# Kernel optimization log

Hardware: AMD Instinct MI355X
Metric: run time of the kernel (lower is better)

The kernel has to match this reference:

```python
import jax, jax.numpy as jnp
import numpy as np

K, D_AMB, D_LAT = 16, 512, 10   # k clusters, ambient dim D, latent dim d
B = 16384                       # batch size
LAMB = 0.01                     # objective regularization weight (default)


def setup_inputs() -> dict:
    key = jax.random.key(0)
    k1, k2, k3 = jax.random.split(key, 3)
    std = 0.1 / np.sqrt(D_AMB)  # reset_parameters: normal(0, 0.1/sqrt(D))
    x = jax.random.normal(k1, (B, D_AMB), dtype=jnp.float32)
    Us = (jax.random.normal(k2, (K, D_AMB, D_LAT), dtype=jnp.float32) * std)
    Vs = (jax.random.normal(k3, (K, D_LAT, D_AMB), dtype=jnp.float32) * std)
    return {"x": x, "Us": Us, "Vs": Vs}


def reference(x, Us, Vs):
    # encode: z[k,b,:] = Vs[k] @ x[b]          (k, B, d)
    z = jnp.einsum('kdD,bD->kbd', Vs, x)
    # decode: x_[k,b,:] = Us[k] @ z[k,b]       (k, B, D)
    x_ = jnp.einsum('kDd,kbd->kbD', Us, z)
    # l2_sqr reconstruction loss, reduced over D, transposed to (B, k)
    diff = x[None, :, :] - x_
    loss = jnp.sum(diff * diff, axis=2).T                      # (B, K)
    # subspace regularization per cluster
    reg = 0.5 * (jnp.sum(Us ** 2, axis=(1, 2))
                 + jnp.sum(Vs ** 2, axis=(1, 2)))              # (K,)
    # hard assignment (soft_assign=0): one-hot argmin of detached assign_obj
    assign_obj = jax.lax.stop_gradient(loss + LAMB * reg[None, :])
    c = jax.nn.one_hot(jnp.argmin(assign_obj, axis=1), K, dtype=loss.dtype)
    # objective: mean over batch of c-weighted loss + lamb * c-weighted reg
    loss_term = jnp.mean(jnp.sum(c * loss, axis=1))
    reg_term = LAMB * jnp.mean(jnp.sum(c * reg[None, :], axis=1))
    return loss_term + reg_term
```

## Files before the change

### kernel.cpp

```cpp
#include <hip/hip_runtime.h>


#define KCLUST   16
#define DAMB     512
#define DLAT     10
#define BATCH    16384
#define LAMBDA   0.01f

#define BM       64
#define NTHREADS 512
#define NKS      16
#define NNT      20
#define NBLK     (BATCH / BM)
#define CHB      40960
#define SSTR     84

typedef __attribute__((ext_vector_type(8))) short short8;
typedef __attribute__((ext_vector_type(4))) float f32x4;

__device__ inline short f2bf(float f) {
    unsigned u = __builtin_bit_cast(unsigned, f);
    unsigned r = (u + 0x7FFFu + ((u >> 16) & 1u)) >> 16;
    return (short)r;
}

__global__ __launch_bounds__(256) void setup_k(const float* __restrict__ Us,
                                               const float* __restrict__ Vs,
                                               short* __restrict__ wpack,
                                               float* __restrict__ G,
                                               float* __restrict__ lreg,
                                               unsigned* __restrict__ cnt) {
    int b = blockIdx.x;
    int tid = threadIdx.x;
    if (b == 0 && tid == 0)
        __hip_atomic_store(cnt, 0u, __ATOMIC_RELEASE, __HIP_MEMORY_SCOPE_AGENT);
    if (b < 80) {
        int idx  = b * 256 + tid;
        int ks   = idx / (NNT * 64);
        int rem  = idx % (NNT * 64);
        int nt   = rem / 64;
        int lane = rem % 64;
        int col  = nt * 16 + (lane & 15);
        int cl   = col / 20;
        int c    = col % 20;
        short8 sv;
#pragma unroll
        for (int j = 0; j < 8; ++j) {
            int k = ks * 32 + (lane >> 4) * 8 + j;
            float v;
            if (c < DLAT) v = Vs[(size_t)cl * DLAT * DAMB + c * DAMB + k];
            else          v = Us[(size_t)cl * DAMB * DLAT + k * DLAT + (c - DLAT)];
            sv[j] = f2bf(v);
        }
        *(short8*)&wpack[(size_t)idx * 8] = sv;
    } else {
        __shared__ float red[256];
        int k = b - 80;
        const float* Uk = Us + (size_t)k * DAMB * DLAT;
        const float* Vk = Vs + (size_t)k * DLAT * DAMB;
        float s = 0.f;
        for (int i = tid; i < DAMB * DLAT; i += 256) {
            float a = Uk[i], bb = Vk[i];
            s += a * a + bb * bb;
        }
        red[tid] = s;
        __syncthreads();
        for (int st = 128; st > 0; st >>= 1) {
            if (tid < st) red[tid] += red[tid + st];
            __syncthreads();
        }
        if (tid == 0) lreg[k] = LAMBDA * 0.5f * red[0];
        if (tid < DLAT * DLAT) {
            int i = tid / DLAT, j = tid % DLAT;
            float g = 0.f;
            for (int Dv = 0; Dv < DAMB; ++Dv)
                g += Uk[Dv * DLAT + i] * Uk[Dv * DLAT + j];
            G[k * 100 + tid] = g;
        }
    }
}

__device__ __forceinline__ void gload_lds16(const void* g, void* l) {
    __builtin_amdgcn_global_load_lds(
        (const __attribute__((address_space(1))) unsigned int*)g,
        (__attribute__((address_space(3))) unsigned int*)l, 16, 0, 0);
}

template <int N> __device__ __forceinline__ void waitv() {
    if constexpr (N == 0)      asm volatile("s_waitcnt vmcnt(0)" ::: "memory");
    else if constexpr (N == 5) asm volatile("s_waitcnt vmcnt(5)" ::: "memory");
    __builtin_amdgcn_sched_barrier(0);
}

__global__ __launch_bounds__(NTHREADS) void main_k(const float* __restrict__ x,
                                                   const short* __restrict__ wpack,
                                                   const float* __restrict__ G,
                                                   const float* __restrict__ lreg,
                                                   float* __restrict__ parts,
                                                   unsigned* __restrict__ cnt,
                                                   float* __restrict__ out) {
    __shared__ __align__(16) char a_region[65536];
    __shared__ __align__(16) char b_region[2 * CHB];
    __shared__ float Gs[KCLUST * 100];
    __shared__ float lregs[KCLUST];
    __shared__ float rsqp[BM][8];
    __shared__ float rowsq_s[BM];
    __shared__ int   isLast;

    short* a_lds = (short*)a_region;
    float* sbuf  = (float*)a_region;
    float (*objl)[17] = (float(*)[17])b_region;

    const int tid  = threadIdx.x;
    const int lane = tid & 63;
    const int wv   = tid >> 6;
    const int mw   = wv >> 2;
    const int nw   = wv & 3;
    const int row0 = blockIdx.x * BM;

    {
        const int srow = tid >> 3;
        const int sc   = tid & 7;
        const int mt   = srow >> 4;
        const int rlo  = srow & 15;
        const float* xr = x + (size_t)(row0 + srow) * DAMB;
        float rs = 0.f;
#pragma unroll
        for (int i = 0; i < 8; ++i) {
            int k8 = sc + 8 * i;
            float4 v0 = *(const float4*)(xr + k8 * 8);
            float4 v1 = *(const float4*)(xr + k8 * 8 + 4);
            rs += v0.x * v0.x + v0.y * v0.y + v0.z * v0.z + v0.w * v0.w
                + v1.x * v1.x + v1.y * v1.y + v1.z * v1.z + v1.w * v1.w;
            short8 sv;
            sv[0] = f2bf(v0.x); sv[1] = f2bf(v0.y); sv[2] = f2bf(v0.z); sv[3] = f2bf(v0.w);
            sv[4] = f2bf(v1.x); sv[5] = f2bf(v1.y); sv[6] = f2bf(v1.z); sv[7] = f2bf(v1.w);
            int ks = k8 >> 2, lh = k8 & 3;
            int ln = (lh << 4) | rlo;
            *(short8*)&a_lds[((mt * NKS + ks) * 64 + ln) * 8] = sv;
        }
        rsqp[srow][sc] = rs;
    }
    for (int i = tid; i < KCLUST * 100; i += NTHREADS) Gs[i] = G[i];
    if (tid < KCLUST) lregs[tid] = lreg[tid];
    __syncthreads();
    if (tid < BM) {
        float s = 0.f;
#pragma unroll
        for (int j = 0; j < 8; ++j) s += rsqp[tid][j];
        rowsq_s[tid] = s;
    }

    f32x4 acc[2][5];
#pragma unroll
    for (int m = 0; m < 2; ++m)
#pragma unroll
        for (int j = 0; j < 5; ++j) acc[m][j] = (f32x4)0.f;

    const char* wsrc = (const char*)wpack;
    const int soff = (wv * 5) * 1024 + lane * 16;

#define ISSUE(c) do { \
        const char* s_ = wsrc + (size_t)(c) * CHB + soff; \
        char* d_ = b_region + ((c) & 1) * CHB + soff; \
        gload_lds16(s_ + 0,    d_ + 0); \
        gload_lds16(s_ + 1024, d_ + 1024); \
        gload_lds16(s_ + 2048, d_ + 2048); \
        gload_lds16(s_ + 3072, d_ + 3072); \
        gload_lds16(s_ + 4096, d_ + 4096); \
        __builtin_amdgcn_sched_barrier(0); \
    } while (0)

#define KSTEP(c, VM) do { \
        waitv<VM>(); \
        __builtin_amdgcn_s_barrier(); \
        __builtin_amdgcn_sched_barrier(0); \
        const short* B_ = (const short*)(b_region + ((c) & 1) * CHB); \
        _Pragma("unroll") \
        for (int ksl = 0; ksl < 2; ++ksl) { \
            short8 a0 = *(short8*)&a_lds[(((mw * 2 + 0) * NKS + (c) * 2 + ksl) * 64 + lane) * 8]; \
            short8 a1 = *(short8*)&a_lds[(((mw * 2 + 1) * NKS + (c) * 2 + ksl) * 64 + lane) * 8]; \
            _Pragma("unroll") \
            for (int j = 0; j < 5; ++j) { \
                short8 bf = *(short8*)&B_[((ksl * NNT + nw * 5 + j) * 64 + lane) * 8]; \
                acc[0][j] = __builtin_amdgcn_mfma_f32_16x16x32_bf16(a0, bf, acc[0][j], 0, 0, 0); \
                acc[1][j] = __builtin_amdgcn_mfma_f32_16x16x32_bf16(a1, bf, acc[1][j], 0, 0, 0); \
            } \
        } \
        __builtin_amdgcn_sched_barrier(0); \
        __builtin_amdgcn_s_barrier(); \
        __builtin_amdgcn_sched_barrier(0); \
    } while (0)

    ISSUE(0); ISSUE(1);
    KSTEP(0, 5); ISSUE(2);
    KSTEP(1, 5); ISSUE(3);
    KSTEP(2, 5); ISSUE(4);
    KSTEP(3, 5); ISSUE(5);
    KSTEP(4, 5); ISSUE(6);
    KSTEP(5, 5); ISSUE(7);
    KSTEP(6, 5);
    KSTEP(7, 0);

#undef KSTEP
#undef ISSUE

    const int stro = wv * (16 * SSTR);
#pragma unroll
    for (int m = 0; m < 2; ++m) {
        int rowb = (lane >> 4) * 4;
#pragma unroll
        for (int j = 0; j < 5; ++j) {
            int colb = j * 16 + (lane & 15);
#pragma unroll
            for (int r = 0; r < 4; ++r)
                sbuf[stro + (rowb + r) * SSTR + colb] = acc[m][j][r];
        }
        {
            int rowl = lane >> 2;
            int cl   = lane & 3;
            const float* yy = sbuf + stro + rowl * SSTR + cl * 20;
            float4 v0 = *(const float4*)(yy + 0);
            float4 v1 = *(const float4*)(yy + 4);
            float4 v2 = *(const float4*)(yy + 8);
            float4 v3 = *(const float4*)(yy + 12);
            float4 v4 = *(const float4*)(yy + 16);
            float z[DLAT] = {v0.x, v0.y, v0.z, v0.w, v1.x, v1.y, v1.z, v1.w, v2.x, v2.y};
            float w[DLAT] = {v2.z, v2.w, v3.x, v3.y, v3.z, v3.w, v4.x, v4.y, v4.z, v4.w};
            int kk = nw * 4 + cl;
            const float* Gk = Gs + kk * 100;
            float s = 0.f, wz = 0.f;
#pragma unroll
            for (int a = 0; a < DLAT; ++a) {
                float gz = 0.f;
#pragma unroll
                for (int b2 = 0; b2 < DLAT; ++b2) gz = fmaf(Gk[a * DLAT + b2], z[b2], gz);
                s  = fmaf(z[a], gz, s);
                wz = fmaf(w[a], z[a], wz);
            }
            objl[mw * 32 + m * 16 + rowl][kk] = s - 2.f * wz + lregs[kk];
        }
        __syncthreads();
    }

    if (wv == 0) {
        float mn = objl[lane][0];
#pragma unroll
        for (int k = 1; k < KCLUST; ++k) mn = fminf(mn, objl[lane][k]);
        float v = mn + rowsq_s[lane];
#pragma unroll
        for (int off = 32; off > 0; off >>= 1) v += __shfl_down(v, off);
        if (lane == 0) {
            __hip_atomic_store(&parts[blockIdx.x], v, __ATOMIC_RELEASE,
                               __HIP_MEMORY_SCOPE_AGENT);
            unsigned prev = __hip_atomic_fetch_add(cnt, 1u, __ATOMIC_ACQ_REL,
                                                   __HIP_MEMORY_SCOPE_AGENT);
            isLast = (prev == NBLK - 1);
        }
    }
    __syncthreads();

    if (isLast && wv == 0) {
        float s = 0.f;
#pragma unroll
        for (int q = 0; q < NBLK / 64; ++q)
            s += __hip_atomic_load(&parts[lane + q * 64], __ATOMIC_RELAXED,
                                   __HIP_MEMORY_SCOPE_AGENT);
#pragma unroll
        for (int off = 32; off > 0; off >>= 1) s += __shfl_down(s, off);
        if (lane == 0) out[0] = s * (1.0f / BATCH);
    }
}

extern "C" void kernel_launch(void* const* d_in, const int* in_sizes, int n_in,
                              void* d_out, int out_size, void* d_ws, size_t ws_size,
                              hipStream_t stream) {
    const float* x  = (const float*)d_in[0];
    const float* Us = (const float*)d_in[1];
    const float* Vs = (const float*)d_in[2];
    float* out = (float*)d_out;

    short* wpack   = (short*)d_ws;
    float* G       = (float*)(wpack + NKS * NNT * 64 * 8);
    float* lreg    = G + KCLUST * 100;
    float* parts   = lreg + KCLUST;
    unsigned* cnt  = (unsigned*)(parts + NBLK);

    setup_k<<<96, 256, 0, stream>>>(Us, Vs, wpack, G, lreg, cnt);
    main_k<<<NBLK, NTHREADS, 0, stream>>>(x, wpack, G, lreg, parts, cnt, out);
}
```

Measured before the change: 45.50 us.

## Split fused kernel into pack, GEMM, and epilogue kernels via global intermediates

Splits the single fused kernel into three launches. One packs x to bf16 and computes row norms, one runs the MFMA GEMM reading pre-packed A through direct global-to-LDS loads and writes Y to global memory, and one does the Gram-matrix epilogue, argmin and reduction. The setup kernel also stages Us in LDS for the Gram computation. This is meant to simplify each kernel and free LDS and registers, but it adds two launches and round-trips a 16 MB bf16 copy of x and a 21 MB Y buffer through global memory.

```diff
diff --git a/kernel.cpp b/kernel.cpp
--- a/kernel.cpp
+++ b/kernel.cpp
@@ -6,14 +6,10 @@
 #define DLAT     10
 #define BATCH    16384
 #define LAMBDA   0.01f
-
-#define BM       64
-#define NTHREADS 512
 #define NKS      16
 #define NNT      20
-#define NBLK     (BATCH / BM)
 #define CHB      40960
-#define SSTR     84
+#define NBLK_E   256
 
 typedef __attribute__((ext_vector_type(8))) short short8;
 typedef __attribute__((ext_vector_type(4))) float f32x4;
@@ -30,6 +26,8 @@
                                                float* __restrict__ G,
                                                float* __restrict__ lreg,
                                                unsigned* __restrict__ cnt) {
+    __shared__ float Ul[DAMB * DLAT];
+    __shared__ float red[256];
     int b = blockIdx.x;
     int tid = threadIdx.x;
     if (b == 0 && tid == 0)
@@ -54,13 +52,13 @@
         }
         *(short8*)&wpack[(size_t)idx * 8] = sv;
     } else {
-        __shared__ float red[256];
         int k = b - 80;
         const float* Uk = Us + (size_t)k * DAMB * DLAT;
         const float* Vk = Vs + (size_t)k * DLAT * DAMB;
         float s = 0.f;
         for (int i = tid; i < DAMB * DLAT; i += 256) {
             float a = Uk[i], bb = Vk[i];
+            Ul[i] = a;
             s += a * a + bb * bb;
         }
         red[tid] = s;
@@ -73,10 +71,44 @@
         if (tid < DLAT * DLAT) {
             int i = tid / DLAT, j = tid % DLAT;
             float g = 0.f;
-            for (int Dv = 0; Dv < DAMB; ++Dv)
-                g += Uk[Dv * DLAT + i] * Uk[Dv * DLAT + j];
+#pragma unroll 8
+            for (int d = 0; d < DAMB; ++d)
+                g = fmaf(Ul[d * DLAT + i], Ul[d * DLAT + j], g);
             G[k * 100 + tid] = g;
         }
+    }
+}
+
+__global__ __launch_bounds__(256) void pack_a(const float* __restrict__ x,
+                                              short* __restrict__ apack,
+                                              float* __restrict__ rowsq) {
+    __shared__ float rsq[16][16];
+    const int mt   = blockIdx.x;
+    const int srow = threadIdx.x >> 4;
+    const int sc   = threadIdx.x & 15;
+    const float* xr = x + ((size_t)mt * 16 + srow) * DAMB;
+    float rs = 0.f;
+#pragma unroll
+    for (int i = 0; i < 4; ++i) {
+        int k8 = sc + 16 * i;
+        float4 v0 = *(const float4*)(xr + k8 * 8);
+        float4 v1 = *(const float4*)(xr + k8 * 8 + 4);
+        rs += v0.x * v0.x + v0.y * v0.y + v0.z * v0.z + v0.w * v0.w
+            + v1.x * v1.x + v1.y * v1.y + v1.z * v1.z + v1.w * v1.w;
+        short8 sv;
+        sv[0] = f2bf(v0.x); sv[1] = f2bf(v0.y); sv[2] = f2bf(v0.z); sv[3] = f2bf(v0.w);
+        sv[4] = f2bf(v1.x); sv[5] = f2bf(v1.y); sv[6] = f2bf(v1.z); sv[7] = f2bf(v1.w);
+        int ks = k8 >> 2, lh = k8 & 3;
+        int ln = (lh << 4) | srow;
+        *(short8*)&apack[(size_t)(((mt * NKS + ks) * 64 + ln)) * 8] = sv;
+    }
+    rsq[srow][sc] = rs;
+    __syncthreads();
+    if (threadIdx.x < 16) {
+        float s = 0.f;
+#pragma unroll
+        for (int j = 0; j < 16; ++j) s += rsq[threadIdx.x][j];
+        rowsq[mt * 16 + threadIdx.x] = s;
     }
 }
 
@@ -92,77 +124,31 @@
     __builtin_amdgcn_sched_barrier(0);
 }
 
-__global__ __launch_bounds__(NTHREADS) void main_k(const float* __restrict__ x,
-                                                   const short* __restrict__ wpack,
-                                                   const float* __restrict__ G,
-                                                   const float* __restrict__ lreg,
-                                                   float* __restrict__ parts,
-                                                   unsigned* __restrict__ cnt,
-                                                   float* __restrict__ out) {
-    __shared__ __align__(16) char a_region[65536];
-    __shared__ __align__(16) char b_region[2 * CHB];
-    __shared__ float Gs[KCLUST * 100];
-    __shared__ float lregs[KCLUST];
-    __shared__ float rsqp[BM][8];
-    __shared__ float rowsq_s[BM];
-    __shared__ int   isLast;
-
-    short* a_lds = (short*)a_region;
-    float* sbuf  = (float*)a_region;
-    float (*objl)[17] = (float(*)[17])b_region;
+__global__ __launch_bounds__(512) void gemm_k(const short* __restrict__ apack,
+                                              const short* __restrict__ wpack,
+                                              float* __restrict__ Y) {
+    __shared__ __align__(16) char a_lds[65536];
+    __shared__ __align__(16) char b_lds[2 * CHB];
 
     const int tid  = threadIdx.x;
     const int lane = tid & 63;
     const int wv   = tid >> 6;
     const int mw   = wv >> 2;
     const int nw   = wv & 3;
-    const int row0 = blockIdx.x * BM;
-
-    {
-        const int srow = tid >> 3;
-        const int sc   = tid & 7;
-        const int mt   = srow >> 4;
-        const int rlo  = srow & 15;
-        const float* xr = x + (size_t)(row0 + srow) * DAMB;
-        float rs = 0.f;
-#pragma unroll
-        for (int i = 0; i < 8; ++i) {
-            int k8 = sc + 8 * i;
-            float4 v0 = *(const float4*)(xr + k8 * 8);
-            float4 v1 = *(const float4*)(xr + k8 * 8 + 4);
-            rs += v0.x * v0.x + v0.y * v0.y + v0.z * v0.z + v0.w * v0.w
-                + v1.x * v1.x + v1.y * v1.y + v1.z * v1.z + v1.w * v1.w;
-            short8 sv;
-            sv[0] = f2bf(v0.x); sv[1] = f2bf(v0.y); sv[2] = f2bf(v0.z); sv[3] = f2bf(v0.w);
-            sv[4] = f2bf(v1.x); sv[5] = f2bf(v1.y); sv[6] = f2bf(v1.z); sv[7] = f2bf(v1.w);
-            int ks = k8 >> 2, lh = k8 & 3;
-            int ln = (lh << 4) | rlo;
-            *(short8*)&a_lds[((mt * NKS + ks) * 64 + ln) * 8] = sv;
-        }
-        rsqp[srow][sc] = rs;
-    }
-    for (int i = tid; i < KCLUST * 100; i += NTHREADS) Gs[i] = G[i];
-    if (tid < KCLUST) lregs[tid] = lreg[tid];
-    __syncthreads();
-    if (tid < BM) {
-        float s = 0.f;
-#pragma unroll
-        for (int j = 0; j < 8; ++j) s += rsqp[tid][j];
-        rowsq_s[tid] = s;
-    }
-
-    f32x4 acc[2][5];
-#pragma unroll
-    for (int m = 0; m < 2; ++m)
-#pragma unroll
-        for (int j = 0; j < 5; ++j) acc[m][j] = (f32x4)0.f;
+    const int row0 = blockIdx.x * 64;
+
+    const char* asrc = (const char*)apack + (size_t)blockIdx.x * 65536;
+#pragma unroll
+    for (int r = 0; r < 8; ++r)
+        gload_lds16(asrc + r * 8192 + tid * 16, a_lds + r * 8192 + tid * 16);
+    __builtin_amdgcn_sched_barrier(0);
 
     const char* wsrc = (const char*)wpack;
     const int soff = (wv * 5) * 1024 + lane * 16;
 
 #define ISSUE(c) do { \
         const char* s_ = wsrc + (size_t)(c) * CHB + soff; \
-        char* d_ = b_region + ((c) & 1) * CHB + soff; \
+        char* d_ = b_lds + ((c) & 1) * CHB + soff; \
         gload_lds16(s_ + 0,    d_ + 0); \
         gload_lds16(s_ + 1024, d_ + 1024); \
         gload_lds16(s_ + 2048, d_ + 2048); \
@@ -171,15 +157,21 @@
         __builtin_amdgcn_sched_barrier(0); \
     } while (0)
 
+    f32x4 acc[2][5];
+#pragma unroll
+    for (int m = 0; m < 2; ++m)
+#pragma unroll
+        for (int j = 0; j < 5; ++j) acc[m][j] = (f32x4)0.f;
+
 #define KSTEP(c, VM) do { \
         waitv<VM>(); \
         __builtin_amdgcn_s_barrier(); \
         __builtin_amdgcn_sched_barrier(0); \
-        const short* B_ = (const short*)(b_region + ((c) & 1) * CHB); \
+        const short* B_ = (const short*)(b_lds + ((c) & 1) * CHB); \
         _Pragma("unroll") \
         for (int ksl = 0; ksl < 2; ++ksl) { \
-            short8 a0 = *(short8*)&a_lds[(((mw * 2 + 0) * NKS + (c) * 2 + ksl) * 64 + lane) * 8]; \
-            short8 a1 = *(short8*)&a_lds[(((mw * 2 + 1) * NKS + (c) * 2 + ksl) * 64 + lane) * 8]; \
+            short8 a0 = *(short8*)&a_lds[((((mw * 2 + 0) * NKS + (c) * 2 + ksl) * 64 + lane)) * 16]; \
+            short8 a1 = *(short8*)&a_lds[((((mw * 2 + 1) * NKS + (c) * 2 + ksl) * 64 + lane)) * 16]; \
             _Pragma("unroll") \
             for (int j = 0; j < 5; ++j) { \
                 short8 bf = *(short8*)&B_[((ksl * NNT + nw * 5 + j) * 64 + lane) * 8]; \
@@ -205,70 +197,90 @@
 #undef KSTEP
 #undef ISSUE
 
-    const int stro = wv * (16 * SSTR);
 #pragma unroll
     for (int m = 0; m < 2; ++m) {
-        int rowb = (lane >> 4) * 4;
-#pragma unroll
-        for (int j = 0; j < 5; ++j) {
-            int colb = j * 16 + (lane & 15);
+        int rowb = row0 + mw * 32 + m * 16 + (lane >> 4) * 4;
+        int colb = (nw * 5) * 16 + (lane & 15);
+#pragma unroll
+        for (int j = 0; j < 5; ++j)
 #pragma unroll
             for (int r = 0; r < 4; ++r)
-                sbuf[stro + (rowb + r) * SSTR + colb] = acc[m][j][r];
-        }
-        {
-            int rowl = lane >> 2;
-            int cl   = lane & 3;
-            const float* yy = sbuf + stro + rowl * SSTR + cl * 20;
-            float4 v0 = *(const float4*)(yy + 0);
-            float4 v1 = *(const float4*)(yy + 4);
-            float4 v2 = *(const float4*)(yy + 8);
-            float4 v3 = *(const float4*)(yy + 12);
-            float4 v4 = *(const float4*)(yy + 16);
-            float z[DLAT] = {v0.x, v0.y, v0.z, v0.w, v1.x, v1.y, v1.z, v1.w, v2.x, v2.y};
-            float w[DLAT] = {v2.z, v2.w, v3.x, v3.y, v3.z, v3.w, v4.x, v4.y, v4.z, v4.w};
-            int kk = nw * 4 + cl;
-            const float* Gk = Gs + kk * 100;
-            float s = 0.f, wz = 0.f;
-#pragma unroll
-            for (int a = 0; a < DLAT; ++a) {
-                float gz = 0.f;
-#pragma unroll
-                for (int b2 = 0; b2 < DLAT; ++b2) gz = fmaf(Gk[a * DLAT + b2], z[b2], gz);
-                s  = fmaf(z[a], gz, s);
-                wz = fmaf(w[a], z[a], wz);
-            }
-            objl[mw * 32 + m * 16 + rowl][kk] = s - 2.f * wz + lregs[kk];
-        }
-        __syncthreads();
-    }
-
-    if (wv == 0) {
-        float mn = objl[lane][0];
-#pragma unroll
-        for (int k = 1; k < KCLUST; ++k) mn = fminf(mn, objl[lane][k]);
-        float v = mn + rowsq_s[lane];
+                Y[(size_t)(rowb + r) * 320 + colb + j * 16] = acc[m][j][r];
+    }
+}
+
+__global__ __launch_bounds__(256) void epi_k(const float* __restrict__ Y,
+                                             const float* __restrict__ G,
+                                             const float* __restrict__ lreg,
+                                             const float* __restrict__ rowsq,
+                                             float* __restrict__ parts,
+                                             unsigned* __restrict__ cnt,
+                                             float* __restrict__ out) {
+    __shared__ float Gs[KCLUST * 100];
+    __shared__ float lr[KCLUST];
+    __shared__ float rmin[64];
+    __shared__ int   isLast;
+
+    const int tid = threadIdx.x;
+    for (int i = tid; i < KCLUST * 100; i += 256) Gs[i] = G[i];
+    if (tid < KCLUST) lr[tid] = lreg[tid];
+    __syncthreads();
+
+    const int row = blockIdx.x * 64 + (tid >> 2);
+    const int cg  = tid & 3;
+    const float* yb = Y + (size_t)row * 320 + cg * 80;
+
+    float m = 3.4e38f;
+#pragma unroll
+    for (int q = 0; q < 4; ++q) {
+        const float* yy = yb + q * 20;
+        float4 v0 = *(const float4*)(yy + 0);
+        float4 v1 = *(const float4*)(yy + 4);
+        float4 v2 = *(const float4*)(yy + 8);
+        float4 v3 = *(const float4*)(yy + 12);
+        float4 v4 = *(const float4*)(yy + 16);
+        float z[DLAT] = {v0.x, v0.y, v0.z, v0.w, v1.x, v1.y, v1.z, v1.w, v2.x, v2.y};
+        float w[DLAT] = {v2.z, v2.w, v3.x, v3.y, v3.z, v3.w, v4.x, v4.y, v4.z, v4.w};
+        int kk = cg * 4 + q;
+        const float* Gk = Gs + kk * 100;
+        float s = 0.f, wz = 0.f;
+#pragma unroll
+        for (int a = 0; a < DLAT; ++a) {
+            float gz = 0.f;
+#pragma unroll
+            for (int b2 = 0; b2 < DLAT; ++b2) gz = fmaf(Gk[a * DLAT + b2], z[b2], gz);
+            s  = fmaf(z[a], gz, s);
+            wz = fmaf(w[a], z[a], wz);
+        }
+        m = fminf(m, s - 2.f * wz + lr[kk]);
+    }
+    m = fminf(m, __shfl_xor(m, 1));
+    m = fminf(m, __shfl_xor(m, 2));
+    if (cg == 0) rmin[tid >> 2] = m + rowsq[row];
+    __syncthreads();
+
+    if (tid < 64) {
+        float v = rmin[tid];
 #pragma unroll
         for (int off = 32; off > 0; off >>= 1) v += __shfl_down(v, off);
-        if (lane == 0) {
+        if (tid == 0) {
             __hip_atomic_store(&parts[blockIdx.x], v, __ATOMIC_RELEASE,
                                __HIP_MEMORY_SCOPE_AGENT);
             unsigned prev = __hip_atomic_fetch_add(cnt, 1u, __ATOMIC_ACQ_REL,
                                                    __HIP_MEMORY_SCOPE_AGENT);
-            isLast = (prev == NBLK - 1);
+            isLast = (prev == NBLK_E - 1);
         }
     }
     __syncthreads();
-
-    if (isLast && wv == 0) {
+    if (isLast && tid < 64) {
         float s = 0.f;
 #pragma unroll
-        for (int q = 0; q < NBLK / 64; ++q)
-            s += __hip_atomic_load(&parts[lane + q * 64], __ATOMIC_RELAXED,
+        for (int q = 0; q < NBLK_E / 64; ++q)
+            s += __hip_atomic_load(&parts[tid + q * 64], __ATOMIC_RELAXED,
                                    __HIP_MEMORY_SCOPE_AGENT);
 #pragma unroll
         for (int off = 32; off > 0; off >>= 1) s += __shfl_down(s, off);
-        if (lane == 0) out[0] = s * (1.0f / BATCH);
+        if (tid == 0) out[0] = s * (1.0f / BATCH);
     }
 }
 
@@ -280,12 +292,18 @@
     const float* Vs = (const float*)d_in[2];
     float* out = (float*)d_out;
 
-    short* wpack   = (short*)d_ws;
-    float* G       = (float*)(wpack + NKS * NNT * 64 * 8);
-    float* lreg    = G + KCLUST * 100;
-    float* parts   = lreg + KCLUST;
-    unsigned* cnt  = (unsigned*)(parts + NBLK);
+    char* wsb = (char*)d_ws;
+    short* wpack = (short*)wsb;
+    short* apack = (short*)(wsb + 327680);
+    float* Y     = (float*)(wsb + 17104896);
+    float* G     = (float*)(wsb + 38076416);
+    float* lreg  = G + KCLUST * 100;
+    float* rowsq = lreg + KCLUST;
+    float* parts = rowsq + BATCH;
+    unsigned* cnt = (unsigned*)(parts + NBLK_E);
 
     setup_k<<<96, 256, 0, stream>>>(Us, Vs, wpack, G, lreg, cnt);
-    main_k<<<NBLK, NTHREADS, 0, stream>>>(x, wpack, G, lreg, parts, cnt, out);
-}
+    pack_a<<<BATCH / 16, 256, 0, stream>>>(x, apack, rowsq);
+    gemm_k<<<BATCH / 64, 512, 0, stream>>>(apack, wpack, Y);
+    epi_k<<<NBLK_E, 256, 0, stream>>>(Y, G, lreg, rowsq, parts, cnt, out);
+}
```

Result: slower. 55.43 us (+21.8%).
